# Optimization experiments

Measured on AMD Instinct MI355X. Metric: run time of the kernel, lower is better.

The kernel has to match this reference:

```python
import jax, jax.numpy as jnp
import numpy as np

B, N, C, D, O = 32, 512, 16, 256, 256


def setup_inputs() -> dict:
    key = jax.random.key(0)
    k1, k2, k3, k4, k5, k6 = jax.random.split(key, 6)
    std = 1.0 / np.sqrt(D)
    nodes = jax.random.normal(k1, (B, N, D), jnp.float32)
    children = jax.random.randint(k2, (B, N, C), 0, N)  # 0 == no-child sentinel
    w_t = jax.random.normal(k3, (D, O), jnp.float32) * std
    w_l = jax.random.normal(k4, (D, O), jnp.float32) * std
    w_r = jax.random.normal(k5, (D, O), jnp.float32) * std
    conv = jax.random.normal(k6, (O,), jnp.float32) * np.sqrt(2.0 / D)
    return {"nodes": nodes, "w_t": w_t, "w_l": w_l, "w_r": w_r, "conv": conv,
            "children": children}


def _coefs(children):
    # children: (B, N, C) int. Returns coef (B, N, C+1, 3) = stack(c_t, c_r, c_l).
    b, n, c = children.shape
    y = c + 1
    has_child = jnp.minimum(children, 1).astype(jnp.float32)          # (B,N,C)
    mask = jnp.concatenate([jnp.zeros((b, n, 1), jnp.float32), has_child], axis=2)  # (B,N,Y)
    # eta_t: 1 at slot 0 (parent), 0 elsewhere
    c_t = jnp.concatenate([jnp.ones((b, n, 1), jnp.float32),
                           jnp.zeros((b, n, c), jnp.float32)], axis=2)
    # eta_r
    ns = jnp.count_nonzero(children, axis=2).astype(jnp.float32)[..., None]  # (B,N,1)
    p = jnp.arange(-1.0, c, dtype=jnp.float32)                        # (Y,): -1,0,1,...
    child_idx = p * mask                                              # (B,N,Y)
    singles = (jnp.arange(y) == 1).astype(jnp.float32) * 0.5          # (Y,)
    denom = jnp.where(ns == 1.0, 1.0, ns - 1.0)                       # safe divide
    c_r = jnp.where(ns == 1.0,
                    jnp.broadcast_to(singles, mask.shape),
                    (1.0 - c_t) * (child_idx / denom))
    # eta_l
    c_l = (1.0 - c_t) * (1.0 - c_r) * mask
    return jnp.stack([c_t, c_r, c_l], axis=3)                         # (B,N,Y,3)


def reference(nodes, w_t, w_l, w_r, conv, children):
    b, n, d = nodes.shape
    c = children.shape[2]
    # gather children embeddings: child_emb[b,i,j] = nodes[b, children[b,i,j]]
    flat_idx = children.reshape(b, n * c)
    child_emb = jnp.take_along_axis(nodes, flat_idx[:, :, None], axis=1)
    child_emb = child_emb.reshape(b, n, c, d)
    child_emb = jnp.where((children == 0)[..., None], 0.0, child_emb)
    tree = jnp.concatenate([nodes[:, :, None, :], child_emb], axis=2)  # (B,N,Y,D)
    coef = _coefs(children)                                            # (B,N,Y,3)
    weights = jnp.stack([w_t, w_r, w_l], axis=0)                       # (3,D,O)
    agg = jnp.einsum('bnyd,bnyk->bnkd', tree, coef)                    # (B,N,3,D)
    res = jnp.einsum('bnkd,kdo->bno', agg, weights)                    # (B,N,O)
    return jax.nn.leaky_relu(res + conv, negative_slope=0.01)
```

## Files before the change

kernel.cpp:

```cpp
#include <hip/hip_runtime.h>
#include <hip/hip_bf16.h>
#include <stdint.h>

#define CC 16
#define OO 256
#define NSLAB 24
#define SLAB_ELS 2048
#define MT_ELS (NSLAB * SLAB_ELS)
#define AGG_ELS (16384 * 768)
#define NB_ELS  (16384 * 256)

typedef __attribute__((ext_vector_type(8))) short bf16x8;
typedef __attribute__((ext_vector_type(4))) float f32x4;

__device__ __forceinline__ unsigned short f2bf(float x) {
    unsigned u = __builtin_bit_cast(unsigned, x);
    u += 0x7FFFu + ((u >> 16) & 1u);
    return (unsigned short)(u >> 16);
}

__device__ __forceinline__ void st_bf4(unsigned short* p, float4 v) {
    uint2 u;
    u.x = (unsigned)f2bf(v.x) | ((unsigned)f2bf(v.y) << 16);
    u.y = (unsigned)f2bf(v.z) | ((unsigned)f2bf(v.w) << 16);
    *(uint2*)p = u;
}

__device__ __forceinline__ void cp16(const void* g, void* l) {
    __builtin_amdgcn_global_load_lds(
        (const __attribute__((address_space(1))) unsigned int*)g,
        (__attribute__((address_space(3))) unsigned int*)l, 16, 0, 0);
}

__global__ __launch_bounds__(256) void prep(
    const float* __restrict__ nodes, const float* __restrict__ wt,
    const float* __restrict__ wrp, const float* __restrict__ wl,
    unsigned short* __restrict__ nb, unsigned short* __restrict__ wsb) {

    __shared__ unsigned short T[256 * 40];
    const int p = blockIdx.x;
    const int tid = threadIdx.x;

    if (p < 2048) {
        const size_t t = (size_t)p * 256 + tid;
        const float4* s = (const float4*)nodes + t * 2;
        float4 a = s[0], b = s[1];
        uint4 u;
        u.x = (unsigned)f2bf(a.x) | ((unsigned)f2bf(a.y) << 16);
        u.y = (unsigned)f2bf(a.z) | ((unsigned)f2bf(a.w) << 16);
        u.z = (unsigned)f2bf(b.x) | ((unsigned)f2bf(b.y) << 16);
        u.w = (unsigned)f2bf(b.z) | ((unsigned)f2bf(b.w) << 16);
        *(uint4*)(nb + t * 8) = u;
        return;
    }
    const int slab = p - 2048;
    const int n = tid;
#pragma unroll
    for (int kk = 0; kk < 32; ++kk) {
        const int k = slab * 32 + kk;
        const float* s = (k < 256) ? wt : ((k < 512) ? wrp : wl);
        T[n * 40 + kk] = f2bf(s[(k & 255) * OO + n]);
    }
    __syncthreads();
    uint4* dst = (uint4*)(wsb + slab * 8192 + n * 32);
    const uint4* src = (const uint4*)&T[n * 40];
#pragma unroll
    for (int q = 0; q < 4; ++q) dst[q] = src[q];
}

__global__ __launch_bounds__(256, 8) void gather(
    const float* __restrict__ nodes, const unsigned short* __restrict__ nb,
    const int* __restrict__ children, unsigned short* __restrict__ agg) {

    const int wave = threadIdx.x >> 6;
    const int lane = threadIdx.x & 63;
    const int p = blockIdx.x;
    const int g = (p & 7) * 512 + (p >> 3);
    const int nf = __builtin_amdgcn_readfirstlane(g * 4 + wave);
    const int brow = nf & ~511;

    const int* chp = children + (nf << 4);
    int cj[CC];
#pragma unroll
    for (int j = 0; j < CC; ++j) cj[j] = chp[j];
    int ns = 0;
#pragma unroll
    for (int j = 0; j < CC; ++j) ns += (cj[j] != 0) ? 1 : 0;
    const float inv_den = (ns > 1) ? 1.0f / (float)(ns - 1) : 0.0f;
    const bool single = (ns == 1);

    const float4* g4 = (const float4*)nodes;
    float4 pt = g4[(size_t)nf * 64 + lane];
    uint2 ec[CC];
#pragma unroll
    for (int j = 0; j < CC; ++j)
        ec[j] = *(const uint2*)(nb + ((size_t)(brow + cj[j]) << 8) + (lane << 2));

    float4 ar = make_float4(0.f, 0.f, 0.f, 0.f);
    float4 al = make_float4(0.f, 0.f, 0.f, 0.f);
#pragma unroll
    for (int j = 0; j < CC; ++j) {
        const float hasf = (cj[j] != 0) ? 1.0f : 0.0f;
        const float crr = single ? ((j == 0) ? 0.5f : 0.0f) : (float)j * inv_den;
        const float cr = crr * hasf;
        const float cl = (1.0f - crr) * hasf;
        const float e0 = __builtin_bit_cast(float, ec[j].x << 16);
        const float e1 = __builtin_bit_cast(float, ec[j].x & 0xFFFF0000u);
        const float e2 = __builtin_bit_cast(float, ec[j].y << 16);
        const float e3 = __builtin_bit_cast(float, ec[j].y & 0xFFFF0000u);
        ar.x += cr * e0; ar.y += cr * e1; ar.z += cr * e2; ar.w += cr * e3;
        al.x += cl * e0; al.y += cl * e1; al.z += cl * e2; al.w += cl * e3;
    }

    const int sl  = lane >> 3;
    const int kwb = (lane & 7) * 4;
    unsigned short* rowp = agg + (size_t)(nf >> 6) * MT_ELS
                               + (size_t)(nf & 63) * 32 + kwb;
    st_bf4(rowp + (size_t)(0  + sl) * SLAB_ELS, pt);
    st_bf4(rowp + (size_t)(8  + sl) * SLAB_ELS, ar);
    st_bf4(rowp + (size_t)(16 + sl) * SLAB_ELS, al);
}

__global__ __launch_bounds__(256, 2) void gemm_ep(
    const unsigned short* __restrict__ agg, const unsigned short* __restrict__ wsb,
    const float* __restrict__ conv, float* __restrict__ out) {

    __shared__ unsigned short Ab[2][SLAB_ELS];
    __shared__ unsigned short Bb[2][4096];

    const int tid  = threadIdx.x;
    const int wave = tid >> 6;
    const int lane = tid & 63;
    const int quad = lane >> 4;
    const int l16  = lane & 15;
    const int x = blockIdx.x & 7;
    const int q = blockIdx.x >> 3;
    const int mtile = x * 32 + (q >> 1);
    const int ntile = q & 1;
    const int wrr = wave >> 1;
    const int wcc = wave & 1;

    const char* aggb = (const char*)agg + (size_t)mtile * (MT_ELS * 2);
    const char* wsbb = (const char*)wsb + ntile * 8192;
    const int toff  = tid * 16;
    const int wbase = (tid & ~63) * 16;

    f32x4 acc[2][4];
#pragma unroll
    for (int mi = 0; mi < 2; ++mi)
#pragma unroll
        for (int ni = 0; ni < 4; ++ni)
            acc[mi][ni] = (f32x4){0.f, 0.f, 0.f, 0.f};

    auto stage = [&](int s, int b) {
        const char* ga = aggb + s * 4096 + toff;
        cp16(ga, (char*)&Ab[b][0] + wbase);
        const char* gb = wsbb + s * 16384 + toff;
        cp16(gb,        (char*)&Bb[b][0] + wbase);
        cp16(gb + 4096, (char*)&Bb[b][0] + wbase + 4096);
    };

    stage(0, 0);
#pragma unroll 1
    for (int s = 0; s < NSLAB; ++s) {
        const int cur = s & 1;
        __syncthreads();
        if (s + 1 < NSLAB) stage(s + 1, cur ^ 1);

        bf16x8 af[2], bfr[4];
#pragma unroll
        for (int mi = 0; mi < 2; ++mi)
            af[mi] = *(const bf16x8*)&Ab[cur][(wrr * 32 + mi * 16 + l16) * 32 + quad * 8];
#pragma unroll
        for (int ni = 0; ni < 4; ++ni)
            bfr[ni] = *(const bf16x8*)&Bb[cur][(wcc * 64 + ni * 16 + l16) * 32 + quad * 8];
#pragma unroll
        for (int mi = 0; mi < 2; ++mi)
#pragma unroll
            for (int ni = 0; ni < 4; ++ni)
                acc[mi][ni] = __builtin_amdgcn_mfma_f32_16x16x32_bf16(
                    af[mi], bfr[ni], acc[mi][ni], 0, 0, 0);
    }

#pragma unroll
    for (int ni = 0; ni < 4; ++ni) {
        const int col = ntile * 128 + wcc * 64 + ni * 16 + l16;
        const float cv = conv[col];
#pragma unroll
        for (int mi = 0; mi < 2; ++mi) {
#pragma unroll
            for (int r = 0; r < 4; ++r) {
                const int row = mtile * 64 + wrr * 32 + mi * 16 + quad * 4 + r;
                float v = acc[mi][ni][r] + cv;
                v = (v > 0.f) ? v : 0.01f * v;
                out[(size_t)row * OO + col] = v;
            }
        }
    }
}

extern "C" void kernel_launch(void* const* d_in, const int* in_sizes, int n_in,
                              void* d_out, int out_size, void* d_ws, size_t ws_size,
                              hipStream_t stream) {
    const float* nodes    = (const float*)d_in[0];
    const float* w_t      = (const float*)d_in[1];
    const float* w_l      = (const float*)d_in[2];
    const float* w_r      = (const float*)d_in[3];
    const float* conv     = (const float*)d_in[4];
    const int*   children = (const int*)d_in[5];

    unsigned short* agg = (unsigned short*)d_ws;
    unsigned short* wsb = agg + AGG_ELS;
    unsigned short* nbb = wsb + 768 * 256;

    prep<<<2048 + 24, 256, 0, stream>>>(nodes, w_t, w_r, w_l, nbb, wsb);
    gather<<<4096, 256, 0, stream>>>(nodes, nbb, children, agg);
    gemm_ep<<<512, 256, 0, stream>>>(agg, wsb, conv, (float*)d_out);
}
```

Baseline: 111.0 us.

## Write bf16 parent rows directly into row-major agg and drop fp32 reload

The prep kernel now writes bf16 node embeddings straight into the first 256 columns of a row-major agg buffer, so the gather kernel no longer re-reads fp32 nodes or writes the parent slice. Gather reads child embeddings from agg with a 1536-byte row stride and computes the left aggregate as the sum of present children minus the right aggregate, cutting one multiply-accumulate chain. The GEMM loads A tiles from row-major rows (64 bytes per row per slab) instead of pre-tiled slabs, which may reduce coalescing of A loads. Prep blocks are also remapped in an interleaved order.

```diff
diff --git a/kernel.cpp b/kernel.cpp
--- a/kernel.cpp
+++ b/kernel.cpp
@@ -5,10 +5,7 @@
 #define CC 16
 #define OO 256
 #define NSLAB 24
-#define SLAB_ELS 2048
-#define MT_ELS (NSLAB * SLAB_ELS)
 #define AGG_ELS (16384 * 768)
-#define NB_ELS  (16384 * 256)
 
 typedef __attribute__((ext_vector_type(8))) short bf16x8;
 typedef __attribute__((ext_vector_type(4))) float f32x4;
@@ -19,13 +16,6 @@
     return (unsigned short)(u >> 16);
 }
 
-__device__ __forceinline__ void st_bf4(unsigned short* p, float4 v) {
-    uint2 u;
-    u.x = (unsigned)f2bf(v.x) | ((unsigned)f2bf(v.y) << 16);
-    u.y = (unsigned)f2bf(v.z) | ((unsigned)f2bf(v.w) << 16);
-    *(uint2*)p = u;
-}
-
 __device__ __forceinline__ void cp16(const void* g, void* l) {
     __builtin_amdgcn_global_load_lds(
         (const __attribute__((address_space(1))) unsigned int*)g,
@@ -35,14 +25,15 @@
 __global__ __launch_bounds__(256) void prep(
     const float* __restrict__ nodes, const float* __restrict__ wt,
     const float* __restrict__ wrp, const float* __restrict__ wl,
-    unsigned short* __restrict__ nb, unsigned short* __restrict__ wsb) {
+    unsigned short* __restrict__ agg, unsigned short* __restrict__ wsb) {
 
     __shared__ unsigned short T[256 * 40];
     const int p = blockIdx.x;
     const int tid = threadIdx.x;
 
     if (p < 2048) {
-        const size_t t = (size_t)p * 256 + tid;
+        const int pp = (p & 7) * 256 + (p >> 3);
+        const size_t t = (size_t)pp * 256 + tid;
         const float4* s = (const float4*)nodes + t * 2;
         float4 a = s[0], b = s[1];
         uint4 u;
@@ -50,7 +41,8 @@
         u.y = (unsigned)f2bf(a.z) | ((unsigned)f2bf(a.w) << 16);
         u.z = (unsigned)f2bf(b.x) | ((unsigned)f2bf(b.y) << 16);
         u.w = (unsigned)f2bf(b.z) | ((unsigned)f2bf(b.w) << 16);
-        *(uint4*)(nb + t * 8) = u;
+        const size_t row = t >> 5;
+        *(uint4*)(agg + row * 768 + (t & 31) * 8) = u;
         return;
     }
     const int slab = p - 2048;
@@ -69,7 +61,6 @@
 }
 
 __global__ __launch_bounds__(256, 8) void gather(
-    const float* __restrict__ nodes, const unsigned short* __restrict__ nb,
     const int* __restrict__ children, unsigned short* __restrict__ agg) {
 
     const int wave = threadIdx.x >> 6;
@@ -89,43 +80,43 @@
     const float inv_den = (ns > 1) ? 1.0f / (float)(ns - 1) : 0.0f;
     const bool single = (ns == 1);
 
-    const float4* g4 = (const float4*)nodes;
-    float4 pt = g4[(size_t)nf * 64 + lane];
     uint2 ec[CC];
 #pragma unroll
     for (int j = 0; j < CC; ++j)
-        ec[j] = *(const uint2*)(nb + ((size_t)(brow + cj[j]) << 8) + (lane << 2));
+        ec[j] = *(const uint2*)(agg + (size_t)(brow + cj[j]) * 768 + lane * 4);
 
     float4 ar = make_float4(0.f, 0.f, 0.f, 0.f);
-    float4 al = make_float4(0.f, 0.f, 0.f, 0.f);
+    float4 as = make_float4(0.f, 0.f, 0.f, 0.f);
 #pragma unroll
     for (int j = 0; j < CC; ++j) {
         const float hasf = (cj[j] != 0) ? 1.0f : 0.0f;
         const float crr = single ? ((j == 0) ? 0.5f : 0.0f) : (float)j * inv_den;
         const float cr = crr * hasf;
-        const float cl = (1.0f - crr) * hasf;
         const float e0 = __builtin_bit_cast(float, ec[j].x << 16);
         const float e1 = __builtin_bit_cast(float, ec[j].x & 0xFFFF0000u);
         const float e2 = __builtin_bit_cast(float, ec[j].y << 16);
         const float e3 = __builtin_bit_cast(float, ec[j].y & 0xFFFF0000u);
-        ar.x += cr * e0; ar.y += cr * e1; ar.z += cr * e2; ar.w += cr * e3;
-        al.x += cl * e0; al.y += cl * e1; al.z += cl * e2; al.w += cl * e3;
-    }
-
-    const int sl  = lane >> 3;
-    const int kwb = (lane & 7) * 4;
-    unsigned short* rowp = agg + (size_t)(nf >> 6) * MT_ELS
-                               + (size_t)(nf & 63) * 32 + kwb;
-    st_bf4(rowp + (size_t)(0  + sl) * SLAB_ELS, pt);
-    st_bf4(rowp + (size_t)(8  + sl) * SLAB_ELS, ar);
-    st_bf4(rowp + (size_t)(16 + sl) * SLAB_ELS, al);
+        ar.x += cr * e0;   ar.y += cr * e1;   ar.z += cr * e2;   ar.w += cr * e3;
+        as.x += hasf * e0; as.y += hasf * e1; as.z += hasf * e2; as.w += hasf * e3;
+    }
+    const float4 al = make_float4(as.x - ar.x, as.y - ar.y,
+                                  as.z - ar.z, as.w - ar.w);
+
+    unsigned short* rowp = agg + (size_t)nf * 768;
+    uint2 u;
+    u.x = (unsigned)f2bf(ar.x) | ((unsigned)f2bf(ar.y) << 16);
+    u.y = (unsigned)f2bf(ar.z) | ((unsigned)f2bf(ar.w) << 16);
+    *(uint2*)(rowp + 256 + lane * 4) = u;
+    u.x = (unsigned)f2bf(al.x) | ((unsigned)f2bf(al.y) << 16);
+    u.y = (unsigned)f2bf(al.z) | ((unsigned)f2bf(al.w) << 16);
+    *(uint2*)(rowp + 512 + lane * 4) = u;
 }
 
 __global__ __launch_bounds__(256, 2) void gemm_ep(
     const unsigned short* __restrict__ agg, const unsigned short* __restrict__ wsb,
     const float* __restrict__ conv, float* __restrict__ out) {
 
-    __shared__ unsigned short Ab[2][SLAB_ELS];
+    __shared__ unsigned short Ab[2][2048];
     __shared__ unsigned short Bb[2][4096];
 
     const int tid  = threadIdx.x;
@@ -140,10 +131,11 @@
     const int wrr = wave >> 1;
     const int wcc = wave & 1;
 
-    const char* aggb = (const char*)agg + (size_t)mtile * (MT_ELS * 2);
+    const char* aggb = (const char*)agg + (size_t)mtile * (64 * 1536);
     const char* wsbb = (const char*)wsb + ntile * 8192;
     const int toff  = tid * 16;
     const int wbase = (tid & ~63) * 16;
+    const char* arow = aggb + (size_t)(tid >> 2) * 1536 + (tid & 3) * 16;
 
     f32x4 acc[2][4];
 #pragma unroll
@@ -153,8 +145,7 @@
             acc[mi][ni] = (f32x4){0.f, 0.f, 0.f, 0.f};
 
     auto stage = [&](int s, int b) {
-        const char* ga = aggb + s * 4096 + toff;
-        cp16(ga, (char*)&Ab[b][0] + wbase);
+        cp16(arow + s * 64, (char*)&Ab[b][0] + wbase);
         const char* gb = wsbb + s * 16384 + toff;
         cp16(gb,        (char*)&Bb[b][0] + wbase);
         cp16(gb + 4096, (char*)&Bb[b][0] + wbase + 4096);
@@ -211,9 +202,8 @@
 
     unsigned short* agg = (unsigned short*)d_ws;
     unsigned short* wsb = agg + AGG_ELS;
-    unsigned short* nbb = wsb + 768 * 256;
-
-    prep<<<2048 + 24, 256, 0, stream>>>(nodes, w_t, w_r, w_l, nbb, wsb);
-    gather<<<4096, 256, 0, stream>>>(nodes, nbb, children, agg);
+
+    prep<<<2048 + 24, 256, 0, stream>>>(nodes, w_t, w_r, w_l, agg, wsb);
+    gather<<<4096, 256, 0, stream>>>(children, agg);
     gemm_ep<<<512, 256, 0, stream>>>(agg, wsb, conv, (float*)d_out);
 }
```

Result: no change. 110.3 us (-0.6%).
